# Kernel optimization log

Hardware: AMD Instinct MI355X
Metric: run time of the kernel (lower is better)

Reference implementation:

```python
import jax, jax.numpy as jnp
import numpy as np

HEADS = 16
DHEAD = 128
B, S, DMODEL = 2, 2048, 2048


def setup_inputs() -> dict:
    key = jax.random.key(0)
    k1, k2, k3 = jax.random.split(key, 3)
    x = jax.random.normal(k1, (B, S, DMODEL), dtype=jnp.float32)
    # Linear weights, stored as [in, out] so forward is x @ w (no bias).
    w_in = jax.random.normal(k2, (DMODEL, 3 * HEADS * DHEAD), dtype=jnp.float32) * (DMODEL ** -0.5)
    w_out = jax.random.normal(k3, (HEADS * DHEAD, DMODEL), dtype=jnp.float32) * ((HEADS * DHEAD) ** -0.5)
    # Causal mask: True = masked (strictly upper triangular), broadcast over batch & heads.
    mask = jnp.triu(jnp.ones((S, S), dtype=jnp.bool_), k=1)[None, None, :, :]
    return {"x": x, "w_in": w_in, "w_out": w_out, "mask": mask}


def reference(x, w_in, w_out, mask):
    b, s, _ = x.shape
    # Fused QKV projection: [b,s,3*H*dh] -> [b,s,H,3*dh] -> chunk into q,k,v [b,s,H,dh]
    projected = (x @ w_in).reshape(b, s, HEADS, 3 * DHEAD)
    q, k, v = jnp.split(projected, 3, axis=-1)
    # Scores [b,H,l,L], scaled by 1/sqrt(dhead)
    scale = 1.0 / (DHEAD ** 0.5)
    a = jnp.einsum("blhd,bLhd->bhlL", q, k) * scale
    a = jnp.where(mask, -jnp.inf, a)
    a = jax.nn.softmax(a, axis=-1)
    # Weighted values -> [b,l,H,dh] -> flatten heads -> output projection
    out = jnp.einsum("bhlL,bLhd->blhd", a, v).reshape(b, s, HEADS * DHEAD)
    return out @ w_out
```

## Files before the change

### kernel.cpp

```cpp
#include <hip/hip_runtime.h>

#define HD    16
#define DH    128
#define BB    2
#define SS    2048
#define DM    2048
#define NQKV  6144
#define MTOT  4096

typedef short   bfx8  __attribute__((ext_vector_type(8)));
typedef float   f32x4 __attribute__((ext_vector_type(4)));

__device__ __forceinline__ unsigned short f2bf(float f) {
  union { float f; unsigned int u; } c; c.f = f;
  unsigned int u = c.u + 0x7FFFu + ((c.u >> 16) & 1u);
  return (unsigned short)(u >> 16);
}

__device__ __forceinline__ void gload_lds16(const unsigned short* g, unsigned short* l) {
  __builtin_amdgcn_global_load_lds(
      (const __attribute__((address_space(1))) unsigned int*)g,
      (__attribute__((address_space(3))) unsigned int*)l, 16, 0, 0);
}

#define BARS() do { __builtin_amdgcn_sched_barrier(0); __builtin_amdgcn_s_barrier(); \
                    __builtin_amdgcn_sched_barrier(0); } while (0)
#define VMCNT8() do { asm volatile("s_waitcnt vmcnt(8)" ::: "memory"); \
                      __builtin_amdgcn_sched_barrier(0); } while (0)

__global__ __launch_bounds__(256) void f32_to_bf16_k(const float* __restrict__ in,
                                                     unsigned short* __restrict__ out, int n4) {
  int i = (blockIdx.x * 256 + threadIdx.x);
  if (i >= n4) return;
  const float4 v = *(const float4*)(in + (size_t)i * 4);
  ushort4 o;
  o.x = f2bf(v.x); o.y = f2bf(v.y); o.z = f2bf(v.z); o.w = f2bf(v.w);
  *(ushort4*)(out + (size_t)i * 4) = o;
}

__global__ __launch_bounds__(256) void transpose_f32_bf16_k(const float* __restrict__ in,
                                                            unsigned short* __restrict__ out,
                                                            int R, int C) {
  __shared__ float t[32][33];
  const int c0 = blockIdx.x * 32, r0 = blockIdx.y * 32;
  const int tx = threadIdx.x & 31, ty = threadIdx.x >> 5;
#pragma unroll
  for (int i = 0; i < 4; i++) {
    int r = r0 + ty + i * 8;
    t[ty + i * 8][tx] = in[(size_t)r * C + c0 + tx];
  }
  __syncthreads();
#pragma unroll
  for (int i = 0; i < 4; i++) {
    int c = c0 + ty + i * 8;
    out[(size_t)c * R + r0 + tx] = f2bf(t[tx][ty + i * 8]);
  }
}

__global__ __launch_bounds__(512, 2) void gemm256_qkv_k(const unsigned short* __restrict__ A,
                                                        const unsigned short* __restrict__ Bt,
                                                        unsigned short* __restrict__ Qg,
                                                        unsigned short* __restrict__ Kg,
                                                        unsigned short* __restrict__ Vg,
                                                        int K) {
  __shared__ __align__(16) unsigned short Asb[2][256 * 64];
  __shared__ __align__(16) unsigned short Bsb[2][256 * 64];
  const int tid = threadIdx.x;
  const int lane = tid & 63, wid = tid >> 6;
  const int wr = wid >> 2, wc = wid & 3;
  const int cbase = lane & 15, rgrp = lane >> 4;
  const int bid = (int)blockIdx.x;
  const int id = (bid & 7) * 48 + (bid >> 3);
  const int nb = id >> 4, mb = id & 15;
  const size_t m0 = (size_t)mb * 256, n0 = (size_t)nb * 256;
  const int nkt = K >> 6;

#define STAGE_HALF(u_, half_) do {                                                      \
    const int uc_ = ((u_) < nkt ? (u_) : (nkt - 1));                                    \
    unsigned short* ldsb_ = (((half_) < 2) ? &Asb[(u_) & 1][0] : &Bsb[(u_) & 1][0])     \
                            + ((half_) & 1) * (128 * 64);                               \
    const unsigned short* gb_ = (((half_) < 2)                                          \
        ? A  + (m0 + (size_t)((half_) & 1) * 128) * (size_t)K                           \
        : Bt + (n0 + (size_t)((half_) & 1) * 128) * (size_t)K);                         \
    _Pragma("unroll")                                                                   \
    for (int ld_ = 0; ld_ < 2; ld_++) {                                                 \
      const int idx_ = ld_ * 512 + tid;                                                 \
      const int row_ = idx_ >> 3, seg_ = idx_ & 7;                                      \
      gload_lds16(gb_ + (size_t)row_ * K + uc_ * 64 +                                   \
                      (((seg_ * 16) ^ ((row_ & 7) << 4)) >> 1),                         \
                  ldsb_ + idx_ * 8);                                                    \
    } } while (0)

  const int axor = (cbase & 7) << 4;
  int a_off[2], b_off[2];
#pragma unroll
  for (int ks = 0; ks < 2; ks++) {
    a_off[ks] = ((wr * 128 + cbase) * 128 + ((ks * 64 + rgrp * 16) ^ axor)) >> 1;
    b_off[ks] = ((wc * 64 + cbase) * 128 + ((ks * 64 + rgrp * 16) ^ axor)) >> 1;
  }

#define RD_A03(dst_, p_) do { _Pragma("unroll")                                          \
    for (int mf_ = 0; mf_ < 4; mf_++) { _Pragma("unroll")                                \
      for (int ks_ = 0; ks_ < 2; ks_++)                                                  \
        dst_[mf_][ks_] = *(const bfx8*)((p_) + a_off[ks_] + mf_ * 1024); } } while (0)
#define RD_A47(dst_, p_) do { _Pragma("unroll")                                          \
    for (int mf_ = 0; mf_ < 4; mf_++) { _Pragma("unroll")                                \
      for (int ks_ = 0; ks_ < 2; ks_++)                                                  \
        dst_[mf_][ks_] = *(const bfx8*)((p_) + a_off[ks_] + (mf_ + 4) * 1024); } } while (0)
#define RD_B01(dst_, p_) do { _Pragma("unroll")                                          \
    for (int nf_ = 0; nf_ < 2; nf_++) { _Pragma("unroll")                                \
      for (int ks_ = 0; ks_ < 2; ks_++)                                                  \
        dst_[nf_][ks_] = *(const bfx8*)((p_) + b_off[ks_] + nf_ * 1024); } } while (0)
#define RD_B23(dst_, p_) do { _Pragma("unroll")                                          \
    for (int nf_ = 0; nf_ < 2; nf_++) { _Pragma("unroll")                                \
      for (int ks_ = 0; ks_ < 2; ks_++)                                                  \
        dst_[nf_][ks_] = *(const bfx8*)((p_) + b_off[ks_] + (nf_ + 2) * 1024); } } while (0)

#define MFMA_Q(mo_, no_, AF_, BF_) do {                                                  \
    __builtin_amdgcn_s_setprio(1);                                                      \
    _Pragma("unroll")                                                                    \
    for (int mf_ = 0; mf_ < 4; mf_++) { _Pragma("unroll")                                \
      for (int nf_ = 0; nf_ < 2; nf_++) { _Pragma("unroll")                              \
        for (int ks_ = 0; ks_ < 2; ks_++)                                                \
          acc[mf_ + (mo_)][nf_ + (no_)] = __builtin_amdgcn_mfma_f32_16x16x32_bf16(       \
              AF_[mf_][ks_], BF_[nf_][ks_], acc[mf_ + (mo_)][nf_ + (no_)], 0, 0, 0); } } \
    __builtin_amdgcn_s_setprio(0); } while (0)

  f32x4 acc[8][4];
  const f32x4 z = {0.f, 0.f, 0.f, 0.f};
#pragma unroll
  for (int mf = 0; mf < 8; mf++)
#pragma unroll
    for (int nf = 0; nf < 4; nf++) acc[mf][nf] = z;

  STAGE_HALF(0, 2); STAGE_HALF(0, 3); STAGE_HALF(0, 0); STAGE_HALF(0, 1);
  STAGE_HALF(1, 2); STAGE_HALF(1, 3); STAGE_HALF(1, 0); STAGE_HALF(1, 1);
  VMCNT8();
  BARS();
  bfx8 a03A[4][2], b01A[2][2], a03B[4][2], b01B[2][2];
  RD_A03(a03A, &Asb[0][0]);
  RD_B01(b01A, &Bsb[0][0]);

#define TILE_BODY(u_, A03_, B01_, NA03_, NB01_) do {                                     \
    const unsigned short* As_  = &Asb[(u_) & 1][0];                                      \
    const unsigned short* Bs_  = &Bsb[(u_) & 1][0];                                      \
    const unsigned short* Asn_ = &Asb[((u_) + 1) & 1][0];                                \
    const unsigned short* Bsn_ = &Bsb[((u_) + 1) & 1][0];                                \
    bfx8 a47[4][2], b23[2][2];                                                           \
                     \
    RD_B23(b23, Bs_);                                                                    \
    BARS();                                                                              \
    MFMA_Q(0, 0, A03_, B01_);                                                            \
    BARS();                                                 \
                       \
    RD_A47(a47, As_);                                                                    \
    STAGE_HALF((u_) + 2, 2); STAGE_HALF((u_) + 2, 3);                                    \
    BARS();                                                                              \
    MFMA_Q(0, 2, A03_, b23);                                                             \
    BARS();                                                 \
                                        \
    STAGE_HALF((u_) + 2, 0); STAGE_HALF((u_) + 2, 1);                                    \
    BARS();                                                                              \
    MFMA_Q(4, 0, a47, B01_);                                                             \
    BARS();                                                                              \
      \
                             \
    VMCNT8();                                                                            \
    BARS();                                                                              \
    RD_A03(NA03_, Asn_);                                                                 \
    RD_B01(NB01_, Bsn_);                                                                 \
    MFMA_Q(4, 2, a47, b23);                                                              \
    BARS();                                                                              \
  } while (0)

#pragma unroll 1
  for (int u = 0; u < nkt; u += 2) {
    TILE_BODY(u,     a03A, b01A, a03B, b01B);
    TILE_BODY(u + 1, a03B, b01B, a03A, b01A);
  }
#undef TILE_BODY
#undef STAGE_HALF

#pragma unroll
  for (int mf = 0; mf < 8; mf++)
#pragma unroll
    for (int nf = 0; nf < 4; nf++) {
      const int nn = (int)n0 + wc * 64 + nf * 16;
      const int h = nn / 384, tt = (nn >> 7) % 3;
      const int d = (nn & 127) + cbase;
      const int row0 = (int)m0 + wr * 128 + mf * 16 + rgrp * 4;
      const int bb = row0 >> 11;
      const int s0 = row0 & 2047;
      if (tt == 2) {
        ushort4 v;
        v.x = f2bf(acc[mf][nf][0]); v.y = f2bf(acc[mf][nf][1]);
        v.z = f2bf(acc[mf][nf][2]); v.w = f2bf(acc[mf][nf][3]);
        *(ushort4*)(Vg + ((size_t)(bb * HD + h) * DH + d) * SS + s0) = v;
      } else {
        unsigned short* dst = (tt == 0 ? Qg : Kg);
#pragma unroll
        for (int r = 0; r < 4; r++)
          dst[((size_t)(bb * HD + h) * SS + s0 + r) * DH + d] = f2bf(acc[mf][nf][r]);
      }
    }
}

__global__ __launch_bounds__(256) void gemm_out_k(const unsigned short* __restrict__ A,
                                                  const unsigned short* __restrict__ Bt,
                                                  float* __restrict__ C, int K, int ldc) {
  __shared__ __align__(16) unsigned short As[128 * 32];
  __shared__ __align__(16) unsigned short Bs[128 * 32];
  const int tid = threadIdx.x;
  const int lane = tid & 63, wid = tid >> 6;
  const int wr = wid >> 1, wc = wid & 1;
  const int cbase = lane & 15, rgrp = lane >> 4;
  const size_t m0 = (size_t)blockIdx.y * 128, n0 = (size_t)blockIdx.x * 128;

  f32x4 acc[4][4];
  const f32x4 z = {0.f, 0.f, 0.f, 0.f};
#pragma unroll
  for (int mf = 0; mf < 4; mf++)
#pragma unroll
    for (int nf = 0; nf < 4; nf++) acc[mf][nf] = z;

  const int nkt = K >> 5;
  for (int kt = 0; kt < nkt; ++kt) {
#pragma unroll
    for (int i = 0; i < 2; i++) {
      int idx = i * 256 + tid;
      int row = idx >> 2, cb = idx & 3;
      gload_lds16(A + (m0 + row) * K + (kt * 32 + cb * 8), As + idx * 8);
      gload_lds16(Bt + (n0 + row) * K + (kt * 32 + cb * 8), Bs + idx * 8);
    }
    __syncthreads();
    bfx8 af[4], bfr[4];
#pragma unroll
    for (int mf = 0; mf < 4; mf++)
      af[mf] = *(const bfx8*)(As + (wr * 64 + mf * 16 + cbase) * 32 + rgrp * 8);
#pragma unroll
    for (int nf = 0; nf < 4; nf++)
      bfr[nf] = *(const bfx8*)(Bs + (wc * 64 + nf * 16 + cbase) * 32 + rgrp * 8);
#pragma unroll
    for (int mf = 0; mf < 4; mf++)
#pragma unroll
      for (int nf = 0; nf < 4; nf++)
        acc[mf][nf] = __builtin_amdgcn_mfma_f32_16x16x32_bf16(af[mf], bfr[nf], acc[mf][nf], 0, 0, 0);
    __syncthreads();
  }

#pragma unroll
  for (int mf = 0; mf < 4; mf++)
#pragma unroll
    for (int nf = 0; nf < 4; nf++)
#pragma unroll
      for (int r = 0; r < 4; r++) {
        size_t row = m0 + wr * 64 + mf * 16 + rgrp * 4 + r;
        size_t col = n0 + wc * 64 + nf * 16 + cbase;
        C[row * ldc + col] = acc[mf][nf][r];
      }
}

__global__ __launch_bounds__(256) void attn_fwd_k(const unsigned short* __restrict__ Qg,
                                                  const unsigned short* __restrict__ Kg,
                                                  const unsigned short* __restrict__ Vg,
                                                  unsigned short* __restrict__ ao) {
  __shared__ __align__(16) unsigned short Klds[2][64 * 128];
  __shared__ __align__(16) unsigned short Vt[2][128 * 64];
  __shared__ __align__(16) unsigned short Plds[4][16 * 64];
  const int tid = threadIdx.x;
  const int lane = tid & 63, wid = tid >> 6;
  const int cbase = lane & 15, rgrp = lane >> 4;
  const int cx = (cbase & 7) << 4;

  const int bid = (int)blockIdx.x;
  const int bh = (bid & 7) * 4 + ((bid >> 3) & 3);
  const int qt = 31 - (bid >> 5);
  const int b = bh >> 4, h = bh & 15;
  const int qbase = qt * 64;

  const unsigned short* qp0 = Qg + (size_t)(b * HD + h) * SS * DH;
  const unsigned short* kp  = Kg + (size_t)(b * HD + h) * SS * DH;
  const unsigned short* vp  = Vg + (size_t)(b * HD + h) * DH * SS;
  const float scale = 0.08838834764831845f;
  const f32x4 z = {0.f, 0.f, 0.f, 0.f};
  const int qi = qbase + wid * 16 + cbase;

  bfx8 qf[4];
  {
    const unsigned short* qp = qp0 + (size_t)qi * DH;
#pragma unroll
    for (int ks = 0; ks < 4; ks++) qf[ks] = *(const bfx8*)(qp + ks * 32 + rgrp * 8);
  }

  float m_run = -1e30f, l_run = 0.f;
  f32x4 o[8];
#pragma unroll
  for (int mb = 0; mb < 8; mb++) o[mb] = z;

#define STAGE_T(t_, s_) do {                                                        \
    const int kvb_ = (t_) * 64;                                                     \
    _Pragma("unroll")                                                               \
    for (int i_ = 0; i_ < 4; i_++) {                                                \
      int idx_ = i_ * 256 + tid;                                                    \
      int r_ = idx_ >> 4, bo_ = (idx_ & 15) * 16;                                   \
      gload_lds16(kp + (size_t)(kvb_ + r_) * DH + ((bo_ ^ ((r_ & 7) << 4)) >> 1),   \
                  &Klds[s_][idx_ * 8]);                                             \
    }                                                                               \
    _Pragma("unroll")                                                               \
    for (int i_ = 0; i_ < 4; i_++) {                                                \
      int idx_ = i_ * 256 + tid;                                                    \
      int d_ = idx_ >> 3, bo_ = (idx_ & 7) * 16;                                    \
      gload_lds16(vp + (size_t)d_ * SS + kvb_ + ((bo_ ^ ((d_ & 7) << 4)) >> 1),     \
                  &Vt[s_][idx_ * 8]);                                               \
    } } while (0)

  const int ntiles = qt + 1;
  STAGE_T(0, 0);
  __syncthreads();

  for (int t = 0; t < ntiles; ++t) {
    const int sel = t & 1;
    if (t + 1 < ntiles) STAGE_T(t + 1, sel ^ 1);
    const unsigned short* Ks_ = &Klds[sel][0];
    const unsigned short* Vs_ = &Vt[sel][0];
    const int kvb = t * 64;

    f32x4 s[4];
#pragma unroll
    for (int mf = 0; mf < 4; mf++) s[mf] = z;
#pragma unroll
    for (int mf = 0; mf < 4; mf++)
#pragma unroll
      for (int ks = 0; ks < 4; ks++) {
        bfx8 kf = *(const bfx8*)(Ks_ + (((mf * 16 + cbase) * 256 + ((ks * 64 + rgrp * 16) ^ cx)) >> 1));
        s[mf] = __builtin_amdgcn_mfma_f32_16x16x32_bf16(kf, qf[ks], s[mf], 0, 0, 0);
      }

    float sv[4][4];
    const bool diag = (t == ntiles - 1);
#pragma unroll
    for (int mf = 0; mf < 4; mf++)
#pragma unroll
      for (int r = 0; r < 4; r++) {
        float v = s[mf][r] * scale;
        if (diag && (kvb + mf * 16 + rgrp * 4 + r > qi)) v = -1e30f;
        sv[mf][r] = v;
      }
    float tm = sv[0][0];
#pragma unroll
    for (int mf = 0; mf < 4; mf++)
#pragma unroll
      for (int r = 0; r < 4; r++) tm = fmaxf(tm, sv[mf][r]);
    tm = fmaxf(tm, __shfl_xor(tm, 16));
    tm = fmaxf(tm, __shfl_xor(tm, 32));
    const float mnew = fmaxf(m_run, tm);
    float p[4][4];
    float rs = 0.f;
#pragma unroll
    for (int mf = 0; mf < 4; mf++)
#pragma unroll
      for (int r = 0; r < 4; r++) { p[mf][r] = __expf(sv[mf][r] - mnew); rs += p[mf][r]; }
    rs += __shfl_xor(rs, 16);
    rs += __shfl_xor(rs, 32);
    const float alpha = __expf(m_run - mnew);
    l_run = l_run * alpha + rs;
    m_run = mnew;
#pragma unroll
    for (int mb = 0; mb < 8; mb++)
#pragma unroll
      for (int r = 0; r < 4; r++) o[mb][r] *= alpha;

#pragma unroll
    for (int mf = 0; mf < 4; mf++)
#pragma unroll
      for (int rr = 0; rr < 2; rr++) {
        unsigned int pp = (unsigned int)f2bf(p[mf][2 * rr]) |
                          ((unsigned int)f2bf(p[mf][2 * rr + 1]) << 16);
        *(unsigned int*)((char*)&Plds[wid][0] +
                         (cbase * 128 + ((mf * 32 + rgrp * 8 + rr * 4) ^ cx))) = pp;
      }
    bfx8 pf[2];
#pragma unroll
    for (int k2 = 0; k2 < 2; k2++)
      pf[k2] = *(const bfx8*)((const char*)&Plds[wid][0] +
                              (cbase * 128 + ((k2 * 64 + rgrp * 16) ^ cx)));

#pragma unroll
    for (int mb = 0; mb < 8; mb++)
#pragma unroll
      for (int k2 = 0; k2 < 2; k2++) {
        bfx8 vf = *(const bfx8*)(Vs_ + (((mb * 16 + cbase) * 128 + ((k2 * 64 + rgrp * 16) ^ cx)) >> 1));
        o[mb] = __builtin_amdgcn_mfma_f32_16x16x32_bf16(vf, pf[k2], o[mb], 0, 0, 0);
      }
    __syncthreads();
  }
#undef STAGE_T

  const float rinv = 1.0f / l_run;
  unsigned short* aop = ao + ((size_t)(b * SS + qi)) * DM + h * DH + rgrp * 4;
#pragma unroll
  for (int mb = 0; mb < 8; mb++) {
    ushort4 v;
    v.x = f2bf(o[mb][0] * rinv); v.y = f2bf(o[mb][1] * rinv);
    v.z = f2bf(o[mb][2] * rinv); v.w = f2bf(o[mb][3] * rinv);
    *(ushort4*)(aop + mb * 16) = v;
  }
}

extern "C" void kernel_launch(void* const* d_in, const int* in_sizes, int n_in,
                              void* d_out, int out_size, void* d_ws, size_t ws_size,
                              hipStream_t stream) {
  (void)in_sizes; (void)n_in; (void)out_size; (void)ws_size;
  const float* x     = (const float*)d_in[0];
  const float* w_in  = (const float*)d_in[1];
  const float* w_out = (const float*)d_in[2];
  float* out = (float*)d_out;

  char* ws = (char*)d_ws;
  unsigned short* Xb  = (unsigned short*)(ws);
  unsigned short* Wit = (unsigned short*)(ws + (16ull << 20));
  unsigned short* Wot = (unsigned short*)(ws + (40ull << 20));
  unsigned short* Qg  = (unsigned short*)(ws + (48ull << 20));
  unsigned short* Kg  = (unsigned short*)(ws + (64ull << 20));
  unsigned short* Vg  = (unsigned short*)(ws + (80ull << 20));
  unsigned short* AO  = (unsigned short*)(ws + (96ull << 20));

  f32_to_bf16_k<<<MTOT * DM / 4 / 256, 256, 0, stream>>>(x, Xb, MTOT * DM / 4);
  transpose_f32_bf16_k<<<dim3(NQKV / 32, DM / 32), 256, 0, stream>>>(w_in, Wit, DM, NQKV);
  transpose_f32_bf16_k<<<dim3(DM / 32, DM / 32), 256, 0, stream>>>(w_out, Wot, DM, DM);
  gemm256_qkv_k<<<384, 512, 0, stream>>>(Xb, Wit, Qg, Kg, Vg, DM);
  attn_fwd_k<<<1024, 256, 0, stream>>>(Qg, Kg, Vg, AO);
  gemm_out_k<<<dim3(DM / 128, MTOT / 128), 256, 0, stream>>>(AO, Wot, out, DM, DM);
}
```

Before: 273.1 us.

## Shrink QKV GEMM N-tile to 192 and restage loads in 64-row chunks

Changes the QKV projection GEMM tile from 256x256 to 256x192, raising the grid from 384 to 512 blocks so the 256 CUs get a more even share of work. The load staging is rewritten into 64-row chunks with a 7-deep vmcnt wait, and the MFMA schedule is regrouped into two 2-column phases plus a final third-column phase with fewer barriers. Each block now gets less reuse of the A tile and more blocks reload A, while the tile uses less LDS and fewer accumulator registers.

```diff
diff --git a/kernel.cpp b/kernel.cpp
--- a/kernel.cpp
+++ b/kernel.cpp
@@ -25,7 +25,7 @@
 
 #define BARS() do { __builtin_amdgcn_sched_barrier(0); __builtin_amdgcn_s_barrier(); \
                     __builtin_amdgcn_sched_barrier(0); } while (0)
-#define VMCNT8() do { asm volatile("s_waitcnt vmcnt(8)" ::: "memory"); \
+#define VMCNT7() do { asm volatile("s_waitcnt vmcnt(7)" ::: "memory"); \
                       __builtin_amdgcn_sched_barrier(0); } while (0)
 
 __global__ __launch_bounds__(256) void f32_to_bf16_k(const float* __restrict__ in,
@@ -64,39 +64,36 @@
                                                         unsigned short* __restrict__ Vg,
                                                         int K) {
   __shared__ __align__(16) unsigned short Asb[2][256 * 64];
-  __shared__ __align__(16) unsigned short Bsb[2][256 * 64];
+  __shared__ __align__(16) unsigned short Bsb[2][192 * 64];
   const int tid = threadIdx.x;
   const int lane = tid & 63, wid = tid >> 6;
   const int wr = wid >> 2, wc = wid & 3;
   const int cbase = lane & 15, rgrp = lane >> 4;
   const int bid = (int)blockIdx.x;
-  const int id = (bid & 7) * 48 + (bid >> 3);
+  const int id = (bid & 7) * 64 + (bid >> 3);
   const int nb = id >> 4, mb = id & 15;
-  const size_t m0 = (size_t)mb * 256, n0 = (size_t)nb * 256;
+  const size_t m0 = (size_t)mb * 256, n0 = (size_t)nb * 192;
   const int nkt = K >> 6;
 
-#define STAGE_HALF(u_, half_) do {                                                      \
+#define STAGE_A64(u_, g_) do {                                                          \
     const int uc_ = ((u_) < nkt ? (u_) : (nkt - 1));                                    \
-    unsigned short* ldsb_ = (((half_) < 2) ? &Asb[(u_) & 1][0] : &Bsb[(u_) & 1][0])     \
-                            + ((half_) & 1) * (128 * 64);                               \
-    const unsigned short* gb_ = (((half_) < 2)                                          \
-        ? A  + (m0 + (size_t)((half_) & 1) * 128) * (size_t)K                           \
-        : Bt + (n0 + (size_t)((half_) & 1) * 128) * (size_t)K);                         \
-    _Pragma("unroll")                                                                   \
-    for (int ld_ = 0; ld_ < 2; ld_++) {                                                 \
-      const int idx_ = ld_ * 512 + tid;                                                 \
-      const int row_ = idx_ >> 3, seg_ = idx_ & 7;                                      \
-      gload_lds16(gb_ + (size_t)row_ * K + uc_ * 64 +                                   \
-                      (((seg_ * 16) ^ ((row_ & 7) << 4)) >> 1),                         \
-                  ldsb_ + idx_ * 8);                                                    \
-    } } while (0)
+    const int r_ = tid >> 3, s_ = tid & 7;                                              \
+    gload_lds16(A + (m0 + (g_) * 64 + r_) * (size_t)K + uc_ * 64 +                      \
+                    (((s_ * 16) ^ ((r_ & 7) << 4)) >> 1),                               \
+                &Asb[(u_) & 1][(g_) * 4096] + tid * 8); } while (0)
+#define STAGE_B64(u_, g_) do {                                                          \
+    const int uc_ = ((u_) < nkt ? (u_) : (nkt - 1));                                    \
+    const int r_ = tid >> 3, s_ = tid & 7;                                              \
+    gload_lds16(Bt + (n0 + (g_) * 64 + r_) * (size_t)K + uc_ * 64 +                     \
+                    (((s_ * 16) ^ ((r_ & 7) << 4)) >> 1),                               \
+                &Bsb[(u_) & 1][(g_) * 4096] + tid * 8); } while (0)
 
   const int axor = (cbase & 7) << 4;
   int a_off[2], b_off[2];
 #pragma unroll
   for (int ks = 0; ks < 2; ks++) {
     a_off[ks] = ((wr * 128 + cbase) * 128 + ((ks * 64 + rgrp * 16) ^ axor)) >> 1;
-    b_off[ks] = ((wc * 64 + cbase) * 128 + ((ks * 64 + rgrp * 16) ^ axor)) >> 1;
+    b_off[ks] = ((wc * 48 + cbase) * 128 + ((ks * 64 + rgrp * 16) ^ axor)) >> 1;
   }
 
 #define RD_A03(dst_, p_) do { _Pragma("unroll")                                          \
@@ -111,65 +108,70 @@
     for (int nf_ = 0; nf_ < 2; nf_++) { _Pragma("unroll")                                \
       for (int ks_ = 0; ks_ < 2; ks_++)                                                  \
         dst_[nf_][ks_] = *(const bfx8*)((p_) + b_off[ks_] + nf_ * 1024); } } while (0)
-#define RD_B23(dst_, p_) do { _Pragma("unroll")                                          \
-    for (int nf_ = 0; nf_ < 2; nf_++) { _Pragma("unroll")                                \
-      for (int ks_ = 0; ks_ < 2; ks_++)                                                  \
-        dst_[nf_][ks_] = *(const bfx8*)((p_) + b_off[ks_] + (nf_ + 2) * 1024); } } while (0)
-
-#define MFMA_Q(mo_, no_, AF_, BF_) do {                                                  \
+#define RD_B2(dst_, p_) do { _Pragma("unroll")                                           \
+    for (int ks_ = 0; ks_ < 2; ks_++)                                                    \
+      dst_[0][ks_] = *(const bfx8*)((p_) + b_off[ks_] + 2 * 1024); } while (0)
+
+#define MFMA_2N(mo_, AF_, BF_) do {                                                      \
     __builtin_amdgcn_s_setprio(1);                                                      \
     _Pragma("unroll")                                                                    \
     for (int mf_ = 0; mf_ < 4; mf_++) { _Pragma("unroll")                                \
       for (int nf_ = 0; nf_ < 2; nf_++) { _Pragma("unroll")                              \
         for (int ks_ = 0; ks_ < 2; ks_++)                                                \
-          acc[mf_ + (mo_)][nf_ + (no_)] = __builtin_amdgcn_mfma_f32_16x16x32_bf16(       \
-              AF_[mf_][ks_], BF_[nf_][ks_], acc[mf_ + (mo_)][nf_ + (no_)], 0, 0, 0); } } \
+          acc[mf_ + (mo_)][nf_] = __builtin_amdgcn_mfma_f32_16x16x32_bf16(               \
+              AF_[mf_][ks_], BF_[nf_][ks_], acc[mf_ + (mo_)][nf_], 0, 0, 0); } }         \
     __builtin_amdgcn_s_setprio(0); } while (0)
 
-  f32x4 acc[8][4];
+  f32x4 acc[8][3];
   const f32x4 z = {0.f, 0.f, 0.f, 0.f};
 #pragma unroll
   for (int mf = 0; mf < 8; mf++)
 #pragma unroll
-    for (int nf = 0; nf < 4; nf++) acc[mf][nf] = z;
-
-  STAGE_HALF(0, 2); STAGE_HALF(0, 3); STAGE_HALF(0, 0); STAGE_HALF(0, 1);
-  STAGE_HALF(1, 2); STAGE_HALF(1, 3); STAGE_HALF(1, 0); STAGE_HALF(1, 1);
-  VMCNT8();
+    for (int nf = 0; nf < 3; nf++) acc[mf][nf] = z;
+
+  STAGE_A64(0, 0); STAGE_A64(0, 1); STAGE_A64(0, 2); STAGE_A64(0, 3);
+  STAGE_B64(0, 0); STAGE_B64(0, 1); STAGE_B64(0, 2);
+  STAGE_A64(1, 0); STAGE_A64(1, 1); STAGE_A64(1, 2); STAGE_A64(1, 3);
+  STAGE_B64(1, 0); STAGE_B64(1, 1); STAGE_B64(1, 2);
+  VMCNT7();
   BARS();
   bfx8 a03A[4][2], b01A[2][2], a03B[4][2], b01B[2][2];
   RD_A03(a03A, &Asb[0][0]);
   RD_B01(b01A, &Bsb[0][0]);
 
-#define TILE_BODY(u_, A03_, B01_, NA03_, NB01_) do {                                     \
+#define TILE_BODY(u_, A03c, B01c, A03n, B01n) do {                                       \
     const unsigned short* As_  = &Asb[(u_) & 1][0];                                      \
     const unsigned short* Bs_  = &Bsb[(u_) & 1][0];                                      \
     const unsigned short* Asn_ = &Asb[((u_) + 1) & 1][0];                                \
     const unsigned short* Bsn_ = &Bsb[((u_) + 1) & 1][0];                                \
-    bfx8 a47[4][2], b23[2][2];                                                           \
+    bfx8 a47[4][2], b2[1][2];                                                            \
+               \
+    RD_A47(a47, As_);                                                                    \
+    STAGE_A64((u_) + 2, 0); STAGE_A64((u_) + 2, 2);                                      \
+    BARS();                                                                              \
+    MFMA_2N(0, A03c, B01c);                                                              \
                      \
-    RD_B23(b23, Bs_);                                                                    \
+    RD_B2(b2, Bs_);                                                                      \
+    STAGE_A64((u_) + 2, 1); STAGE_A64((u_) + 2, 3);                                      \
     BARS();                                                                              \
-    MFMA_Q(0, 0, A03_, B01_);                                                            \
-    BARS();                                                 \
-                       \
-    RD_A47(a47, As_);                                                                    \
-    STAGE_HALF((u_) + 2, 2); STAGE_HALF((u_) + 2, 3);                                    \
+    MFMA_2N(4, a47, B01c);                                                               \
+     \
+                                     \
+    STAGE_B64((u_) + 2, 0); STAGE_B64((u_) + 2, 1); STAGE_B64((u_) + 2, 2);              \
+    VMCNT7();                                                                            \
     BARS();                                                                              \
-    MFMA_Q(0, 2, A03_, b23);                                                             \
-    BARS();                                                 \
-                                        \
-    STAGE_HALF((u_) + 2, 0); STAGE_HALF((u_) + 2, 1);                                    \
-    BARS();                                                                              \
-    MFMA_Q(4, 0, a47, B01_);                                                             \
-    BARS();                                                                              \
-      \
-                             \
-    VMCNT8();                                                                            \
-    BARS();                                                                              \
-    RD_A03(NA03_, Asn_);                                                                 \
-    RD_B01(NB01_, Bsn_);                                                                 \
-    MFMA_Q(4, 2, a47, b23);                                                              \
+    RD_A03(A03n, Asn_);                                                                  \
+    RD_B01(B01n, Bsn_);                                                                  \
+    __builtin_amdgcn_s_setprio(1);                                                      \
+    _Pragma("unroll")                                                                    \
+    for (int mf_ = 0; mf_ < 4; mf_++) { _Pragma("unroll")                                \
+      for (int ks_ = 0; ks_ < 2; ks_++) {                                                \
+        acc[mf_][2] = __builtin_amdgcn_mfma_f32_16x16x32_bf16(                           \
+            A03c[mf_][ks_], b2[0][ks_], acc[mf_][2], 0, 0, 0);                           \
+        acc[mf_ + 4][2] = __builtin_amdgcn_mfma_f32_16x16x32_bf16(                       \
+            a47[mf_][ks_], b2[0][ks_], acc[mf_ + 4][2], 0, 0, 0);                        \
+      } }                                                                                \
+    __builtin_amdgcn_s_setprio(0);                                                      \
     BARS();                                                                              \
   } while (0)
 
@@ -179,13 +181,14 @@
     TILE_BODY(u + 1, a03B, b01B, a03A, b01A);
   }
 #undef TILE_BODY
-#undef STAGE_HALF
+#undef STAGE_A64
+#undef STAGE_B64
 
 #pragma unroll
   for (int mf = 0; mf < 8; mf++)
 #pragma unroll
-    for (int nf = 0; nf < 4; nf++) {
-      const int nn = (int)n0 + wc * 64 + nf * 16;
+    for (int nf = 0; nf < 3; nf++) {
+      const int nn = (int)n0 + wc * 48 + nf * 16;
       const int h = nn / 384, tt = (nn >> 7) % 3;
       const int d = (nn & 127) + cbase;
       const int row0 = (int)m0 + wr * 128 + mf * 16 + rgrp * 4;
@@ -428,7 +431,7 @@
   f32_to_bf16_k<<<MTOT * DM / 4 / 256, 256, 0, stream>>>(x, Xb, MTOT * DM / 4);
   transpose_f32_bf16_k<<<dim3(NQKV / 32, DM / 32), 256, 0, stream>>>(w_in, Wit, DM, NQKV);
   transpose_f32_bf16_k<<<dim3(DM / 32, DM / 32), 256, 0, stream>>>(w_out, Wot, DM, DM);
-  gemm256_qkv_k<<<384, 512, 0, stream>>>(Xb, Wit, Qg, Kg, Vg, DM);
+  gemm256_qkv_k<<<512, 512, 0, stream>>>(Xb, Wit, Qg, Kg, Vg, DM);
   attn_fwd_k<<<1024, 256, 0, stream>>>(Qg, Kg, Vg, AO);
   gemm_out_k<<<dim3(DM / 128, MTOT / 128), 256, 0, stream>>>(AO, Wot, out, DM, DM);
 }
```

Result: faster. 253.8 us (-7.1%).
